# Kernel tuning notes

Measured on AMD Instinct MI355X. Metric: run time of the kernel, lower is better.

The kernel has to match this reference:

```python
import jax, jax.numpy as jnp
import numpy as np

NEG_MASK = -999999.0  # additive mask constant from the original module


def setup_inputs() -> dict:
    key = jax.random.key(0)
    k1, k2, k3, k4 = jax.random.split(key, 4)
    B, P, H, D = 64, 512, 512, 512
    premise_batch = jax.random.normal(k1, (B, P, D), dtype=jnp.float32)
    hypothesis_batch = jax.random.normal(k2, (B, H, D), dtype=jnp.float32)
    premise_mask = jax.random.randint(k3, (B, P), 0, 2, dtype=jnp.int32)
    hypothesis_mask = jax.random.randint(k4, (B, H), 0, 2, dtype=jnp.int32)
    return {
        "premise_batch": premise_batch,
        "premise_mask": premise_mask,
        "hypothesis_batch": hypothesis_batch,
        "hypothesis_mask": hypothesis_mask,
    }


def reference(premise_batch, premise_mask, hypothesis_batch, hypothesis_mask):
    # similarity: [B, P, H]
    sim = jnp.einsum("bpd,bhd->bph", premise_batch, hypothesis_batch)
    # additive -999999 masks, exactly as in the torch source
    hyp_pad = (hypothesis_mask == 0).astype(sim.dtype)[:, None, :]   # [B,1,H]
    pre_pad = (premise_mask == 0).astype(sim.dtype)[:, :, None]      # [B,P,1]
    sim_hyp = sim + NEG_MASK * hyp_pad
    sim_pre = sim + NEG_MASK * pre_pad
    attention_a = jax.nn.softmax(sim_pre, axis=2)  # softmax over hypothesis dim
    attention_b = jax.nn.softmax(sim_hyp, axis=1)  # softmax over premise dim
    attended_premises = jnp.einsum("bph,bhd->bpd", attention_a, hypothesis_batch)
    attended_hypothesis = jnp.einsum("bph,bpd->bhd", attention_b, premise_batch)
    return (attended_premises, attended_hypothesis)
```

## Files before the change

kernel.cpp:

```cpp
#include <hip/hip_runtime.h>
#include <hip/hip_bf16.h>
#include <math.h>

#define NEG_MASK -999999.0f

constexpr int BB = 64, PP = 512, HH = 512, DD = 512;

typedef __bf16 bfrag __attribute__((ext_vector_type(8)));
typedef __bf16 bf4   __attribute__((ext_vector_type(4)));
typedef float  f32x4 __attribute__((ext_vector_type(4)));

#define MFMA(a, b, c) __builtin_amdgcn_mfma_f32_16x16x32_bf16(a, b, c, 0, 0, 0)

__device__ __forceinline__ int swz(int row, int kb) {
  return (row * 64 + kb) ^ ((row & 7) << 4);
}

__global__ __launch_bounds__(256, 2) void sim_mfma(const float* __restrict__ pre,
                                                   const float* __restrict__ hyp,
                                                   float* __restrict__ sim) {
  const int b = blockIdx.z;
  const int p0 = blockIdx.y * 128, h0 = blockIdx.x * 128;
  const float* A  = pre + (size_t)b * PP * DD;
  const float* Bm = hyp + (size_t)b * HH * DD;

  __shared__ char sAh[128 * 64], sAl[128 * 64], sBh[128 * 64], sBl[128 * 64];

  const int t = threadIdx.x;
  const int r = t >> 1, kh = t & 1;
  const int lane = t & 63, wid = t >> 6;
  const int l15 = lane & 15, l4 = lane >> 4;
  const int wr = (wid >> 1) * 64, wc = (wid & 1) * 64;

  f32x4 acc[4][4] = {};

  const float* pA = A  + (size_t)(p0 + r) * DD + kh * 16;
  const float* pB = Bm + (size_t)(h0 + r) * DD + kh * 16;

  for (int kk = 0; kk < DD; kk += 32) {
    f32x4 ra[4], rb[4];
#pragma unroll
    for (int c = 0; c < 4; ++c) {
      ra[c] = *reinterpret_cast<const f32x4*>(pA + kk + c * 4);
      rb[c] = *reinterpret_cast<const f32x4*>(pB + kk + c * 4);
    }
    __syncthreads();
#pragma unroll
    for (int c = 0; c < 4; ++c) {
      const int kb = kh * 32 + c * 8;
      bf4 ah, al, bh, bl;
#pragma unroll
      for (int e = 0; e < 4; ++e) {
        float fa = ra[c][e], fb = rb[c][e];
        __bf16 ha = (__bf16)fa, hb = (__bf16)fb;
        ah[e] = ha; al[e] = (__bf16)(fa - (float)ha);
        bh[e] = hb; bl[e] = (__bf16)(fb - (float)hb);
      }
      *reinterpret_cast<bf4*>(sAh + swz(r, kb)) = ah;
      *reinterpret_cast<bf4*>(sAl + swz(r, kb)) = al;
      *reinterpret_cast<bf4*>(sBh + swz(r, kb)) = bh;
      *reinterpret_cast<bf4*>(sBl + swz(r, kb)) = bl;
    }
    __syncthreads();

    bfrag Ah[4], Al[4], Bh[4], Bl[4];
#pragma unroll
    for (int i = 0; i < 4; ++i) {
      Ah[i] = *reinterpret_cast<const bfrag*>(sAh + swz(wr + i * 16 + l15, l4 * 16));
      Al[i] = *reinterpret_cast<const bfrag*>(sAl + swz(wr + i * 16 + l15, l4 * 16));
      Bh[i] = *reinterpret_cast<const bfrag*>(sBh + swz(wc + i * 16 + l15, l4 * 16));
      Bl[i] = *reinterpret_cast<const bfrag*>(sBl + swz(wc + i * 16 + l15, l4 * 16));
    }
#pragma unroll
    for (int i = 0; i < 4; ++i)
#pragma unroll
      for (int j = 0; j < 4; ++j) {
        acc[i][j] = MFMA(Ah[i], Bh[j], acc[i][j]);
        acc[i][j] = MFMA(Ah[i], Bl[j], acc[i][j]);
        acc[i][j] = MFMA(Al[i], Bh[j], acc[i][j]);
      }
  }

  float* S = sim + (size_t)b * PP * HH;
#pragma unroll
  for (int i = 0; i < 4; ++i)
#pragma unroll
    for (int j = 0; j < 4; ++j)
#pragma unroll
      for (int rr = 0; rr < 4; ++rr)
        S[(size_t)(p0 + wr + i * 16 + l4 * 4 + rr) * HH + h0 + wc + j * 16 + l15] =
            acc[i][j][rr];
}

__global__ __launch_bounds__(256) void stats_rows(const float* __restrict__ sim,
                                                  const int* __restrict__ pmask,
                                                  float* __restrict__ maxA,
                                                  float* __restrict__ sumA) {
  const int wid = threadIdx.x >> 6, lane = threadIdx.x & 63;
  const int row = blockIdx.x * 4 + wid;
  const float* s = sim + (size_t)row * HH + lane * 8;
  const float c = (pmask[row] == 0) ? NEG_MASK : 0.f;

  f32x4 v0 = *reinterpret_cast<const f32x4*>(s);
  f32x4 v1 = *reinterpret_cast<const f32x4*>(s + 4);
  float tv[8] = {v0[0] + c, v0[1] + c, v0[2] + c, v0[3] + c,
                 v1[0] + c, v1[1] + c, v1[2] + c, v1[3] + c};
  float m = tv[0];
#pragma unroll
  for (int e = 1; e < 8; ++e) m = fmaxf(m, tv[e]);
#pragma unroll
  for (int o = 1; o < 64; o <<= 1) m = fmaxf(m, __shfl_xor(m, o, 64));
  float sum = 0.f;
#pragma unroll
  for (int e = 0; e < 8; ++e) sum += __expf(tv[e] - m);
#pragma unroll
  for (int o = 1; o < 64; o <<= 1) sum += __shfl_xor(sum, o, 64);
  if (lane == 0) { maxA[row] = m; sumA[row] = sum; }
}

__global__ __launch_bounds__(256) void stats_cols(const float* __restrict__ sim,
                                                  const int* __restrict__ hmask,
                                                  float* __restrict__ maxB,
                                                  float* __restrict__ sumB) {
  const int b = blockIdx.y;
  const int th = threadIdx.x & 63, seg = threadIdx.x >> 6;
  const int h = blockIdx.x * 64 + th;
  const float* s = sim + (size_t)b * PP * HH + h;
  const float c = (hmask[b * HH + h] == 0) ? NEG_MASK : 0.f;

  __shared__ float red[4][64];

  float m = -3.4e38f;
  for (int p = seg * 128; p < seg * 128 + 128; ++p)
    m = fmaxf(m, s[(size_t)p * HH] + c);
  red[seg][th] = m;
  __syncthreads();
  m = fmaxf(fmaxf(red[0][th], red[1][th]), fmaxf(red[2][th], red[3][th]));

  float sum = 0.f;
  for (int p = seg * 128; p < seg * 128 + 128; ++p)
    sum += __expf((s[(size_t)p * HH] + c) - m);
  __syncthreads();
  red[seg][th] = sum;
  __syncthreads();
  if (seg == 0) {
    maxB[b * HH + h] = m;
    sumB[b * HH + h] = red[0][th] + red[1][th] + red[2][th] + red[3][th];
  }
}

__global__ __launch_bounds__(256, 3) void att_a_mfma(const float* __restrict__ sim,
                                                     const float* __restrict__ hyp,
                                                     const int* __restrict__ pmask,
                                                     const float* __restrict__ maxA,
                                                     const float* __restrict__ sumA,
                                                     float* __restrict__ out) {
  const int b = blockIdx.z;
  const int p0 = blockIdx.y * 128, d0 = blockIdx.x * 128;
  const float* S = sim + (size_t)b * PP * HH;
  const float* V = hyp + (size_t)b * HH * DD;

  __shared__ char sW[128 * 64], sV[128 * 64];

  const int t = threadIdx.x;
  const int lane = t & 63, wid = t >> 6;
  const int l15 = lane & 15, l4 = lane >> 4;
  const int wr = (wid >> 1) * 64, wc = (wid & 1) * 64;

  const int r = t >> 1, kh = t & 1;
  const float cA = (pmask[b * PP + p0 + r] == 0) ? NEG_MASK : 0.f;
  const float mA = maxA[b * PP + p0 + r];

  const int m = t & 31, q = t >> 5;

  f32x4 acc[4][4] = {};

  for (int kk = 0; kk < HH; kk += 32) {
    f32x4 rs[4], rv[4];
#pragma unroll
    for (int c = 0; c < 4; ++c)
      rs[c] = *reinterpret_cast<const f32x4*>(S + (size_t)(p0 + r) * HH + kk + kh * 16 + c * 4);
#pragma unroll
    for (int jj = 0; jj < 4; ++jj)
      rv[jj] = *reinterpret_cast<const f32x4*>(V + (size_t)(kk + q * 4 + jj) * DD + d0 + m * 4);
    __syncthreads();
#pragma unroll
    for (int c = 0; c < 4; ++c) {
      bf4 w;
#pragma unroll
      for (int e = 0; e < 4; ++e)
        w[e] = (__bf16)__expf((rs[c][e] + cA) - mA);
      *reinterpret_cast<bf4*>(sW + swz(r, kh * 32 + c * 8)) = w;
    }
#pragma unroll
    for (int i = 0; i < 4; ++i) {
      bf4 v;
#pragma unroll
      for (int jj = 0; jj < 4; ++jj) v[jj] = (__bf16)rv[jj][i];
      *reinterpret_cast<bf4*>(sV + swz(m * 4 + i, q * 8)) = v;
    }
    __syncthreads();

    bfrag Wf[4], Vf[4];
#pragma unroll
    for (int i = 0; i < 4; ++i) {
      Wf[i] = *reinterpret_cast<const bfrag*>(sW + swz(wr + i * 16 + l15, l4 * 16));
      Vf[i] = *reinterpret_cast<const bfrag*>(sV + swz(wc + i * 16 + l15, l4 * 16));
    }
#pragma unroll
    for (int i = 0; i < 4; ++i)
#pragma unroll
      for (int j = 0; j < 4; ++j)
        acc[i][j] = MFMA(Wf[i], Vf[j], acc[i][j]);
  }

  float* O = out + (size_t)b * PP * DD;
#pragma unroll
  for (int i = 0; i < 4; ++i)
#pragma unroll
    for (int rr = 0; rr < 4; ++rr) {
      const int prow = p0 + wr + i * 16 + l4 * 4 + rr;
      const float inv = 1.f / sumA[b * PP + prow];
#pragma unroll
      for (int j = 0; j < 4; ++j)
        O[(size_t)prow * DD + d0 + wc + j * 16 + l15] = acc[i][j][rr] * inv;
    }
}

__global__ __launch_bounds__(256, 3) void att_b_mfma(const float* __restrict__ sim,
                                                     const float* __restrict__ pre,
                                                     const int* __restrict__ hmask,
                                                     const float* __restrict__ maxB,
                                                     const float* __restrict__ sumB,
                                                     float* __restrict__ out) {
  const int b = blockIdx.z;
  const int h0 = blockIdx.y * 128, d0 = blockIdx.x * 128;
  const float* S = sim + (size_t)b * PP * HH;
  const float* U = pre + (size_t)b * PP * DD;

  __shared__ char sW[128 * 64], sU[128 * 64];

  const int t = threadIdx.x;
  const int lane = t & 63, wid = t >> 6;
  const int l15 = lane & 15, l4 = lane >> 4;
  const int wr = (wid >> 1) * 64, wc = (wid & 1) * 64;

  const int m = t & 31, q = t >> 5;

  float cH[4], mB[4];
#pragma unroll
  for (int i = 0; i < 4; ++i) {
    const int h = h0 + m * 4 + i;
    cH[i] = (hmask[b * HH + h] == 0) ? NEG_MASK : 0.f;
    mB[i] = maxB[b * HH + h];
  }

  f32x4 acc[4][4] = {};

  for (int kk = 0; kk < PP; kk += 32) {
    f32x4 rs[4], ru[4];
#pragma unroll
    for (int jj = 0; jj < 4; ++jj) {
      rs[jj] = *reinterpret_cast<const f32x4*>(S + (size_t)(kk + q * 4 + jj) * HH + h0 + m * 4);
      ru[jj] = *reinterpret_cast<const f32x4*>(U + (size_t)(kk + q * 4 + jj) * DD + d0 + m * 4);
    }
    __syncthreads();
#pragma unroll
    for (int i = 0; i < 4; ++i) {
      bf4 w, u;
#pragma unroll
      for (int jj = 0; jj < 4; ++jj) {
        w[jj] = (__bf16)__expf((rs[jj][i] + cH[i]) - mB[i]);
        u[jj] = (__bf16)ru[jj][i];
      }
      *reinterpret_cast<bf4*>(sW + swz(m * 4 + i, q * 8)) = w;
      *reinterpret_cast<bf4*>(sU + swz(m * 4 + i, q * 8)) = u;
    }
    __syncthreads();

    bfrag Wf[4], Uf[4];
#pragma unroll
    for (int i = 0; i < 4; ++i) {
      Wf[i] = *reinterpret_cast<const bfrag*>(sW + swz(wr + i * 16 + l15, l4 * 16));
      Uf[i] = *reinterpret_cast<const bfrag*>(sU + swz(wc + i * 16 + l15, l4 * 16));
    }
#pragma unroll
    for (int i = 0; i < 4; ++i)
#pragma unroll
      for (int j = 0; j < 4; ++j)
        acc[i][j] = MFMA(Wf[i], Uf[j], acc[i][j]);
  }

  float* O = out + (size_t)b * HH * DD;
#pragma unroll
  for (int i = 0; i < 4; ++i)
#pragma unroll
    for (int rr = 0; rr < 4; ++rr) {
      const int hrow = h0 + wr + i * 16 + l4 * 4 + rr;
      const float inv = 1.f / sumB[b * HH + hrow];
#pragma unroll
      for (int j = 0; j < 4; ++j)
        O[(size_t)hrow * DD + d0 + wc + j * 16 + l15] = acc[i][j][rr] * inv;
    }
}

extern "C" void kernel_launch(void* const* d_in, const int* in_sizes, int n_in,
                              void* d_out, int out_size, void* d_ws, size_t ws_size,
                              hipStream_t stream) {
  const float* pre  = (const float*)d_in[0];
  const int* pmask  = (const int*)d_in[1];
  const float* hyp  = (const float*)d_in[2];
  const int* hmask  = (const int*)d_in[3];

  float* out0 = (float*)d_out;
  float* out1 = out0 + (size_t)BB * PP * DD;

  float* sim  = (float*)d_ws;
  float* maxA = sim + (size_t)BB * PP * HH;
  float* sumA = maxA + BB * PP;
  float* maxB = sumA + BB * PP;
  float* sumB = maxB + BB * HH;

  sim_mfma<<<dim3(HH / 128, PP / 128, BB), 256, 0, stream>>>(pre, hyp, sim);
  stats_rows<<<dim3(BB * PP / 4), 256, 0, stream>>>(sim, pmask, maxA, sumA);
  stats_cols<<<dim3(HH / 64, BB), 256, 0, stream>>>(sim, hmask, maxB, sumB);
  att_a_mfma<<<dim3(DD / 128, PP / 128, BB), 256, 0, stream>>>(sim, hyp, pmask, maxA, sumA, out0);
  att_b_mfma<<<dim3(DD / 128, HH / 128, BB), 256, 0, stream>>>(sim, pre, hmask, maxB, sumB, out1);
}
```

Measured before the change: 438.0 us.

## Pre-transpose inputs to fp16 and stream V tiles via global_load_lds

Adds a transpose-and-convert kernel that writes premise and hypothesis as fp16 in D-major layout. The attention kernels then load V/U tiles directly into LDS with global_load_lds instead of loading fp32 and transposing in registers. The sim tile loads are prefetched one iteration ahead, and all MFMA paths switch from bf16 to fp16 with 16-byte LDS writes. This trades two extra transpose passes and extra workspace for less conversion and shuffle work in the inner loops; fp16 gives more mantissa bits but a narrower range than bf16.

```diff
diff --git a/kernel.cpp b/kernel.cpp
--- a/kernel.cpp
+++ b/kernel.cpp
@@ -6,14 +6,42 @@
 
 constexpr int BB = 64, PP = 512, HH = 512, DD = 512;
 
-typedef __bf16 bfrag __attribute__((ext_vector_type(8)));
-typedef __bf16 bf4   __attribute__((ext_vector_type(4)));
-typedef float  f32x4 __attribute__((ext_vector_type(4)));
-
-#define MFMA(a, b, c) __builtin_amdgcn_mfma_f32_16x16x32_bf16(a, b, c, 0, 0, 0)
+typedef _Float16 h8    __attribute__((ext_vector_type(8)));
+typedef float    f32x4 __attribute__((ext_vector_type(4)));
+typedef float    f32x2 __attribute__((ext_vector_type(2)));
+
+#define MFMA16(a, b, c) __builtin_amdgcn_mfma_f32_16x16x32_f16(a, b, c, 0, 0, 0)
 
 __device__ __forceinline__ int swz(int row, int kb) {
   return (row * 64 + kb) ^ ((row & 7) << 4);
+}
+
+__device__ __forceinline__ void gload16(const void* g, void* l) {
+  __builtin_amdgcn_global_load_lds(
+      (const __attribute__((address_space(1))) unsigned int*)g,
+      (__attribute__((address_space(3))) unsigned int*)l, 16, 0, 0);
+}
+
+__device__ __forceinline__ void inv_swz(int x, int& row, int& kb) {
+  row = ((x >> 7) << 1) | (((x >> 6) & 1) ^ ((x >> 8) & 1));
+  kb = (x & 63) ^ ((row & 3) << 4);
+}
+
+__global__ __launch_bounds__(256) void tcvt(const float* __restrict__ src,
+                                            _Float16* __restrict__ dst) {
+  const int b = blockIdx.z;
+  const int d0 = blockIdx.x * 64, n0 = blockIdx.y * 64;
+  src += (size_t)b * 512 * 512;
+  dst += (size_t)b * 512 * 512;
+  const int dl = threadIdx.x & 63, nch = (threadIdx.x >> 6) * 16;
+  const float* ps = src + (size_t)(n0 + nch) * 512 + d0 + dl;
+  h8 o[2];
+#pragma unroll
+  for (int e = 0; e < 16; ++e)
+    o[e >> 3][e & 7] = (_Float16)ps[(size_t)e * 512];
+  _Float16* pd = dst + (size_t)(d0 + dl) * 512 + n0 + nch;
+  *reinterpret_cast<h8*>(pd) = o[0];
+  *reinterpret_cast<h8*>(pd + 8) = o[1];
 }
 
 __global__ __launch_bounds__(256, 2) void sim_mfma(const float* __restrict__ pre,
@@ -21,10 +49,8 @@
                                                    float* __restrict__ sim) {
   const int b = blockIdx.z;
   const int p0 = blockIdx.y * 128, h0 = blockIdx.x * 128;
-  const float* A  = pre + (size_t)b * PP * DD;
-  const float* Bm = hyp + (size_t)b * HH * DD;
-
-  __shared__ char sAh[128 * 64], sAl[128 * 64], sBh[128 * 64], sBl[128 * 64];
+
+  __shared__ __align__(16) char sAh[8192], sAl[8192], sBh[8192], sBl[8192];
 
   const int t = threadIdx.x;
   const int r = t >> 1, kh = t & 1;
@@ -34,8 +60,8 @@
 
   f32x4 acc[4][4] = {};
 
-  const float* pA = A  + (size_t)(p0 + r) * DD + kh * 16;
-  const float* pB = Bm + (size_t)(h0 + r) * DD + kh * 16;
+  const float* pA = pre + (size_t)b * PP * DD + (size_t)(p0 + r) * DD + kh * 16;
+  const float* pB = hyp + (size_t)b * HH * DD + (size_t)(h0 + r) * DD + kh * 16;
 
   for (int kk = 0; kk < DD; kk += 32) {
     f32x4 ra[4], rb[4];
@@ -45,39 +71,44 @@
       rb[c] = *reinterpret_cast<const f32x4*>(pB + kk + c * 4);
     }
     __syncthreads();
-#pragma unroll
-    for (int c = 0; c < 4; ++c) {
-      const int kb = kh * 32 + c * 8;
-      bf4 ah, al, bh, bl;
+    h8 vah[2], val[2], vbh[2], vbl[2];
+#pragma unroll
+    for (int c = 0; c < 4; ++c)
 #pragma unroll
       for (int e = 0; e < 4; ++e) {
+        const int idx = c * 4 + e;
         float fa = ra[c][e], fb = rb[c][e];
-        __bf16 ha = (__bf16)fa, hb = (__bf16)fb;
-        ah[e] = ha; al[e] = (__bf16)(fa - (float)ha);
-        bh[e] = hb; bl[e] = (__bf16)(fb - (float)hb);
+        _Float16 ha = (_Float16)fa, hb = (_Float16)fb;
+        vah[idx >> 3][idx & 7] = ha;
+        val[idx >> 3][idx & 7] = (_Float16)(fa - (float)ha);
+        vbh[idx >> 3][idx & 7] = hb;
+        vbl[idx >> 3][idx & 7] = (_Float16)(fb - (float)hb);
       }
-      *reinterpret_cast<bf4*>(sAh + swz(r, kb)) = ah;
-      *reinterpret_cast<bf4*>(sAl + swz(r, kb)) = al;
-      *reinterpret_cast<bf4*>(sBh + swz(r, kb)) = bh;
-      *reinterpret_cast<bf4*>(sBl + swz(r, kb)) = bl;
-    }
-    __syncthreads();
-
-    bfrag Ah[4], Al[4], Bh[4], Bl[4];
+    *reinterpret_cast<h8*>(sAh + swz(r, kh * 32)) = vah[0];
+    *reinterpret_cast<h8*>(sAh + swz(r, kh * 32 + 16)) = vah[1];
+    *reinterpret_cast<h8*>(sAl + swz(r, kh * 32)) = val[0];
+    *reinterpret_cast<h8*>(sAl + swz(r, kh * 32 + 16)) = val[1];
+    *reinterpret_cast<h8*>(sBh + swz(r, kh * 32)) = vbh[0];
+    *reinterpret_cast<h8*>(sBh + swz(r, kh * 32 + 16)) = vbh[1];
+    *reinterpret_cast<h8*>(sBl + swz(r, kh * 32)) = vbl[0];
+    *reinterpret_cast<h8*>(sBl + swz(r, kh * 32 + 16)) = vbl[1];
+    __syncthreads();
+
+    h8 Ah[4], Al[4], Bh[4], Bl[4];
 #pragma unroll
     for (int i = 0; i < 4; ++i) {
-      Ah[i] = *reinterpret_cast<const bfrag*>(sAh + swz(wr + i * 16 + l15, l4 * 16));
-      Al[i] = *reinterpret_cast<const bfrag*>(sAl + swz(wr + i * 16 + l15, l4 * 16));
-      Bh[i] = *reinterpret_cast<const bfrag*>(sBh + swz(wc + i * 16 + l15, l4 * 16));
-      Bl[i] = *reinterpret_cast<const bfrag*>(sBl + swz(wc + i * 16 + l15, l4 * 16));
+      Ah[i] = *reinterpret_cast<const h8*>(sAh + swz(wr + i * 16 + l15, l4 * 16));
+      Al[i] = *reinterpret_cast<const h8*>(sAl + swz(wr + i * 16 + l15, l4 * 16));
+      Bh[i] = *reinterpret_cast<const h8*>(sBh + swz(wc + i * 16 + l15, l4 * 16));
+      Bl[i] = *reinterpret_cast<const h8*>(sBl + swz(wc + i * 16 + l15, l4 * 16));
     }
 #pragma unroll
     for (int i = 0; i < 4; ++i)
 #pragma unroll
       for (int j = 0; j < 4; ++j) {
-        acc[i][j] = MFMA(Ah[i], Bh[j], acc[i][j]);
-        acc[i][j] = MFMA(Ah[i], Bl[j], acc[i][j]);
-        acc[i][j] = MFMA(Al[i], Bh[j], acc[i][j]);
+        acc[i][j] = MFMA16(Ah[i], Bh[j], acc[i][j]);
+        acc[i][j] = MFMA16(Ah[i], Bl[j], acc[i][j]);
+        acc[i][j] = MFMA16(Al[i], Bh[j], acc[i][j]);
       }
   }
 
@@ -150,7 +181,7 @@
 }
 
 __global__ __launch_bounds__(256, 3) void att_a_mfma(const float* __restrict__ sim,
-                                                     const float* __restrict__ hyp,
+                                                     const _Float16* __restrict__ hypT,
                                                      const int* __restrict__ pmask,
                                                      const float* __restrict__ maxA,
                                                      const float* __restrict__ sumA,
@@ -158,9 +189,9 @@
   const int b = blockIdx.z;
   const int p0 = blockIdx.y * 128, d0 = blockIdx.x * 128;
   const float* S = sim + (size_t)b * PP * HH;
-  const float* V = hyp + (size_t)b * HH * DD;
-
-  __shared__ char sW[128 * 64], sV[128 * 64];
+  const _Float16* T = hypT + (size_t)b * DD * HH;
+
+  __shared__ __align__(16) char sW[8192], sV[8192];
 
   const int t = threadIdx.x;
   const int lane = t & 63, wid = t >> 6;
@@ -171,47 +202,52 @@
   const float cA = (pmask[b * PP + p0 + r] == 0) ? NEG_MASK : 0.f;
   const float mA = maxA[b * PP + p0 + r];
 
-  const int m = t & 31, q = t >> 5;
+  int row0, kb0, row1, kb1;
+  inv_swz(t * 16, row0, kb0);
+  inv_swz(4096 + t * 16, row1, kb1);
+  const _Float16* srcV0 = T + (size_t)(d0 + row0) * HH + (kb0 >> 1);
+  const _Float16* srcV1 = T + (size_t)(d0 + row1) * HH + (kb1 >> 1);
+  void* lb0 = sV + wid * 1024;
+  void* lb1 = sV + 4096 + wid * 1024;
+
+  const float* pS = S + (size_t)(p0 + r) * HH + kh * 16;
+  f32x4 rs[4];
+#pragma unroll
+  for (int c = 0; c < 4; ++c) rs[c] = *reinterpret_cast<const f32x4*>(pS + c * 4);
 
   f32x4 acc[4][4] = {};
 
   for (int kk = 0; kk < HH; kk += 32) {
-    f32x4 rs[4], rv[4];
+    h8 wv[2];
 #pragma unroll
     for (int c = 0; c < 4; ++c)
-      rs[c] = *reinterpret_cast<const f32x4*>(S + (size_t)(p0 + r) * HH + kk + kh * 16 + c * 4);
-#pragma unroll
-    for (int jj = 0; jj < 4; ++jj)
-      rv[jj] = *reinterpret_cast<const f32x4*>(V + (size_t)(kk + q * 4 + jj) * DD + d0 + m * 4);
-    __syncthreads();
-#pragma unroll
-    for (int c = 0; c < 4; ++c) {
-      bf4 w;
-#pragma unroll
-      for (int e = 0; e < 4; ++e)
-        w[e] = (__bf16)__expf((rs[c][e] + cA) - mA);
-      *reinterpret_cast<bf4*>(sW + swz(r, kh * 32 + c * 8)) = w;
-    }
+#pragma unroll
+      for (int e = 0; e < 4; ++e) {
+        const int idx = c * 4 + e;
+        wv[idx >> 3][idx & 7] = (_Float16)__expf((rs[c][e] + cA) - mA);
+      }
+    __syncthreads();
+    gload16(srcV0 + kk, lb0);
+    gload16(srcV1 + kk, lb1);
+    *reinterpret_cast<h8*>(sW + swz(r, kh * 32)) = wv[0];
+    *reinterpret_cast<h8*>(sW + swz(r, kh * 32 + 16)) = wv[1];
+    __syncthreads();
+    if (kk + 32 < HH) {
+#pragma unroll
+      for (int c = 0; c < 4; ++c)
+        rs[c] = *reinterpret_cast<const f32x4*>(pS + kk + 32 + c * 4);
+    }
+    h8 Wf[4], Vf[4];
 #pragma unroll
     for (int i = 0; i < 4; ++i) {
-      bf4 v;
-#pragma unroll
-      for (int jj = 0; jj < 4; ++jj) v[jj] = (__bf16)rv[jj][i];
-      *reinterpret_cast<bf4*>(sV + swz(m * 4 + i, q * 8)) = v;
-    }
-    __syncthreads();
-
-    bfrag Wf[4], Vf[4];
-#pragma unroll
-    for (int i = 0; i < 4; ++i) {
-      Wf[i] = *reinterpret_cast<const bfrag*>(sW + swz(wr + i * 16 + l15, l4 * 16));
-      Vf[i] = *reinterpret_cast<const bfrag*>(sV + swz(wc + i * 16 + l15, l4 * 16));
+      Wf[i] = *reinterpret_cast<const h8*>(sW + swz(wr + i * 16 + l15, l4 * 16));
+      Vf[i] = *reinterpret_cast<const h8*>(sV + swz(wc + i * 16 + l15, l4 * 16));
     }
 #pragma unroll
     for (int i = 0; i < 4; ++i)
 #pragma unroll
       for (int j = 0; j < 4; ++j)
-        acc[i][j] = MFMA(Wf[i], Vf[j], acc[i][j]);
+        acc[i][j] = MFMA16(Wf[i], Vf[j], acc[i][j]);
   }
 
   float* O = out + (size_t)b * PP * DD;
@@ -228,7 +264,7 @@
 }
 
 __global__ __launch_bounds__(256, 3) void att_b_mfma(const float* __restrict__ sim,
-                                                     const float* __restrict__ pre,
+                                                     const _Float16* __restrict__ preT,
                                                      const int* __restrict__ hmask,
                                                      const float* __restrict__ maxB,
                                                      const float* __restrict__ sumB,
@@ -236,59 +272,69 @@
   const int b = blockIdx.z;
   const int h0 = blockIdx.y * 128, d0 = blockIdx.x * 128;
   const float* S = sim + (size_t)b * PP * HH;
-  const float* U = pre + (size_t)b * PP * DD;
-
-  __shared__ char sW[128 * 64], sU[128 * 64];
+  const _Float16* T = preT + (size_t)b * DD * PP;
+
+  __shared__ __align__(16) char sW[8192], sU[8192];
 
   const int t = threadIdx.x;
   const int lane = t & 63, wid = t >> 6;
   const int l15 = lane & 15, l4 = lane >> 4;
   const int wr = (wid >> 1) * 64, wc = (wid & 1) * 64;
 
-  const int m = t & 31, q = t >> 5;
-
-  float cH[4], mB[4];
-#pragma unroll
-  for (int i = 0; i < 4; ++i) {
-    const int h = h0 + m * 4 + i;
-    cH[i] = (hmask[b * HH + h] == 0) ? NEG_MASK : 0.f;
-    mB[i] = maxB[b * HH + h];
-  }
+  const int hp = t >> 2, kq = t & 3;
+  float cH[2], mB[2];
+#pragma unroll
+  for (int hh = 0; hh < 2; ++hh) {
+    const int h = h0 + hp * 2 + hh;
+    cH[hh] = (hmask[b * HH + h] == 0) ? NEG_MASK : 0.f;
+    mB[hh] = maxB[b * HH + h];
+  }
+
+  int row0, kb0, row1, kb1;
+  inv_swz(t * 16, row0, kb0);
+  inv_swz(4096 + t * 16, row1, kb1);
+  const _Float16* srcU0 = T + (size_t)(d0 + row0) * PP + (kb0 >> 1);
+  const _Float16* srcU1 = T + (size_t)(d0 + row1) * PP + (kb1 >> 1);
+  void* lb0 = sU + wid * 1024;
+  void* lb1 = sU + 4096 + wid * 1024;
+
+  const float* pS0 = S + h0 + hp * 2;
+  f32x2 rw[8];
+#pragma unroll
+  for (int jj = 0; jj < 8; ++jj)
+    rw[jj] = *reinterpret_cast<const f32x2*>(pS0 + (size_t)(kq * 8 + jj) * HH);
 
   f32x4 acc[4][4] = {};
 
   for (int kk = 0; kk < PP; kk += 32) {
-    f32x4 rs[4], ru[4];
-#pragma unroll
-    for (int jj = 0; jj < 4; ++jj) {
-      rs[jj] = *reinterpret_cast<const f32x4*>(S + (size_t)(kk + q * 4 + jj) * HH + h0 + m * 4);
-      ru[jj] = *reinterpret_cast<const f32x4*>(U + (size_t)(kk + q * 4 + jj) * DD + d0 + m * 4);
-    }
-    __syncthreads();
+    h8 w0, w1;
+#pragma unroll
+    for (int jj = 0; jj < 8; ++jj) {
+      w0[jj] = (_Float16)__expf((rw[jj][0] + cH[0]) - mB[0]);
+      w1[jj] = (_Float16)__expf((rw[jj][1] + cH[1]) - mB[1]);
+    }
+    __syncthreads();
+    gload16(srcU0 + kk, lb0);
+    gload16(srcU1 + kk, lb1);
+    *reinterpret_cast<h8*>(sW + swz(hp * 2 + 0, kq * 16)) = w0;
+    *reinterpret_cast<h8*>(sW + swz(hp * 2 + 1, kq * 16)) = w1;
+    __syncthreads();
+    if (kk + 32 < PP) {
+#pragma unroll
+      for (int jj = 0; jj < 8; ++jj)
+        rw[jj] = *reinterpret_cast<const f32x2*>(pS0 + (size_t)(kk + 32 + kq * 8 + jj) * HH);
+    }
+    h8 Wf[4], Uf[4];
 #pragma unroll
     for (int i = 0; i < 4; ++i) {
-      bf4 w, u;
-#pragma unroll
-      for (int jj = 0; jj < 4; ++jj) {
-        w[jj] = (__bf16)__expf((rs[jj][i] + cH[i]) - mB[i]);
-        u[jj] = (__bf16)ru[jj][i];
-      }
-      *reinterpret_cast<bf4*>(sW + swz(m * 4 + i, q * 8)) = w;
-      *reinterpret_cast<bf4*>(sU + swz(m * 4 + i, q * 8)) = u;
-    }
-    __syncthreads();
-
-    bfrag Wf[4], Uf[4];
-#pragma unroll
-    for (int i = 0; i < 4; ++i) {
-      Wf[i] = *reinterpret_cast<const bfrag*>(sW + swz(wr + i * 16 + l15, l4 * 16));
-      Uf[i] = *reinterpret_cast<const bfrag*>(sU + swz(wc + i * 16 + l15, l4 * 16));
+      Wf[i] = *reinterpret_cast<const h8*>(sW + swz(wr + i * 16 + l15, l4 * 16));
+      Uf[i] = *reinterpret_cast<const h8*>(sU + swz(wc + i * 16 + l15, l4 * 16));
     }
 #pragma unroll
     for (int i = 0; i < 4; ++i)
 #pragma unroll
       for (int j = 0; j < 4; ++j)
-        acc[i][j] = MFMA(Wf[i], Uf[j], acc[i][j]);
+        acc[i][j] = MFMA16(Wf[i], Uf[j], acc[i][j]);
   }
 
   float* O = out + (size_t)b * HH * DD;
@@ -315,15 +361,19 @@
   float* out0 = (float*)d_out;
   float* out1 = out0 + (size_t)BB * PP * DD;
 
-  float* sim  = (float*)d_ws;
-  float* maxA = sim + (size_t)BB * PP * HH;
+  float* sim = (float*)d_ws;
+  _Float16* hypT = (_Float16*)(sim + (size_t)BB * PP * HH);
+  _Float16* preT = hypT + (size_t)BB * DD * HH;
+  float* maxA = (float*)(preT + (size_t)BB * DD * PP);
   float* sumA = maxA + BB * PP;
   float* maxB = sumA + BB * PP;
   float* sumB = maxB + BB * HH;
 
+  tcvt<<<dim3(8, 8, BB), 256, 0, stream>>>(hyp, hypT);
+  tcvt<<<dim3(8, 8, BB), 256, 0, stream>>>(pre, preT);
   sim_mfma<<<dim3(HH / 128, PP / 128, BB), 256, 0, stream>>>(pre, hyp, sim);
   stats_rows<<<dim3(BB * PP / 4), 256, 0, stream>>>(sim, pmask, maxA, sumA);
   stats_cols<<<dim3(HH / 64, BB), 256, 0, stream>>>(sim, hmask, maxB, sumB);
-  att_a_mfma<<<dim3(DD / 128, PP / 128, BB), 256, 0, stream>>>(sim, hyp, pmask, maxA, sumA, out0);
-  att_b_mfma<<<dim3(DD / 128, HH / 128, BB), 256, 0, stream>>>(sim, pre, hmask, maxB, sumB, out1);
-}
+  att_a_mfma<<<dim3(DD / 128, PP / 128, BB), 256, 0, stream>>>(sim, hypT, pmask, maxA, sumA, out0);
+  att_b_mfma<<<dim3(DD / 128, HH / 128, BB), 256, 0, stream>>>(sim, preT, hmask, maxB, sumB, out1);
+}
```

New measurement: 494.8 us. 1.13x slower.
